# Kernel tuning notes

Measured on AMD Instinct MI355X. Metric: run time of the kernel, lower is better.

The kernel has to match this reference:

```python
import jax, jax.numpy as jnp
import numpy as np

B, T, H = 2, 2048, 1024
NH = 16
D = H // NH  # head_dim = 64
SCALE = D ** -0.5


def setup_inputs() -> dict:
    key = jax.random.key(0)
    ks = jax.random.split(key, 10)
    s_in = 1.0 / np.sqrt(H)   # torch Linear init scale for fan_in=H
    s_d = 1.0 / np.sqrt(D)
    return {
        "x":  jax.random.normal(ks[0], (B, T, H), jnp.float32),
        # stacked per-head Q/K projections: [NH, H, D] weights, [NH, D] biases
        "Wq": jax.random.uniform(ks[1], (NH, H, D), jnp.float32, -s_in, s_in),
        "bq": jax.random.uniform(ks[2], (NH, D), jnp.float32, -s_in, s_in),
        "Wk": jax.random.uniform(ks[3], (NH, H, D), jnp.float32, -s_in, s_in),
        "bk": jax.random.uniform(ks[4], (NH, D), jnp.float32, -s_in, s_in),
        # shared V projection H->D
        "Wv": jax.random.uniform(ks[5], (H, D), jnp.float32, -s_in, s_in),
        "bv": jax.random.uniform(ks[6], (D,), jnp.float32, -s_in, s_in),
        # out projection D->H
        "Wo": jax.random.uniform(ks[7], (D, H), jnp.float32, -s_d, s_d),
        "bo": jax.random.uniform(ks[8], (H,), jnp.float32, -s_d, s_d),
    }


def reference(x, Wq, bq, Wk, bk, Wv, bv, Wo, bo):
    # shared value projection: [B,T,D]
    v = jnp.einsum('bth,hd->btd', x, Wv) + bv
    # batched per-head Q/K projections: [NH,B,T,D]
    q = jnp.einsum('bth,nhd->nbtd', x, Wq) + bq[:, None, None, :]
    k = jnp.einsum('bth,nhd->nbtd', x, Wk) + bk[:, None, None, :]
    # scaled causal attention scores: [NH,B,T,T]
    scores = jnp.einsum('nbtd,nbsd->nbts', q, k) * SCALE
    causal = jnp.triu(jnp.ones((T, T), bool), k=1)  # True above diagonal
    scores = jnp.where(causal, -jnp.inf, scores)
    weights = jax.nn.softmax(scores, axis=-1)  # dropout is identity in eval
    # shared V attended per head, then mean over heads: [B,T,D]
    mean_head = jnp.einsum('nbts,bsd->btd', weights, v) / NH
    out = jnp.einsum('btd,dh->bth', mean_head, Wo) + bo
    mean_weights = jnp.mean(weights, axis=0)  # [B,T,T]
    return out, mean_weights
```

## Files before the change

### kernel.cpp

```cpp
#include <hip/hip_runtime.h>
#include <hip/hip_bf16.h>

#define B_ 2
#define T_ 2048
#define H_ 1024
#define NH_ 16
#define D_ 64
#define BT_ (B_*T_)
#define SCALE_ 0.125f
#define LOG2E_ 1.4426950408889634f

typedef _Float16 f16x8 __attribute__((ext_vector_type(8)));
typedef float f32x4 __attribute__((ext_vector_type(4)));

#define MFMA(a,b,c) __builtin_amdgcn_mfma_f32_16x16x32_f16((a),(b),(c),0,0,0)
#define EXP2(x) __builtin_amdgcn_exp2f(x)

typedef const __attribute__((address_space(1))) void GV;
typedef __attribute__((address_space(3))) void LV;

__device__ __forceinline__ size_t toff(int r, int c, int C) {
    return (size_t)((r >> 4) * (C >> 5) + (c >> 5)) * 512 + (size_t)(((c & 31) >> 3) * 128 + (r & 15) * 8 + (c & 7));
}
__device__ __forceinline__ f16x8 frag_ld(const _Float16* base, int rt, int kc, int Cc, int l15, int quad) {
    return *(const f16x8*)(base + (size_t)(rt * Cc + kc) * 512 + quad * 128 + l15 * 8);
}

__global__ __launch_bounds__(256) void k_prep(const float* __restrict__ x,
                                              const float* __restrict__ Wq, const float* __restrict__ Wk,
                                              const float* __restrict__ Wv, const float* __restrict__ Wo,
                                              _Float16* __restrict__ xb, _Float16* __restrict__ wqk,
                                              _Float16* __restrict__ wvt, _Float16* __restrict__ wot,
                                              float* __restrict__ mw) {
    int blk = blockIdx.x, tid = threadIdx.x;
    if (blk < 2048) {
        int idx = blk * 256 + tid;
        int t = idx >> 7, h0 = (idx & 127) * 8;
        const float* p = x + ((size_t)t << 10) + h0;
        float4 f0 = *(const float4*)p;
        float4 f1 = *(const float4*)(p + 4);
        f16x8 o;
        o[0]=(_Float16)f0.x; o[1]=(_Float16)f0.y; o[2]=(_Float16)f0.z; o[3]=(_Float16)f0.w;
        o[4]=(_Float16)f1.x; o[5]=(_Float16)f1.y; o[6]=(_Float16)f1.z; o[7]=(_Float16)f1.w;
        *(f16x8*)(xb + toff(t, h0, 1024)) = o;
    } else if (blk < 2560) {
        int idx = (blk - 2048) * 256 + tid;
        int head = idx >> 13;
        int rem = idx & 8191;
        int h = rem >> 3;
        int d0 = (rem & 7) * 8;
        const float* pq = Wq + ((size_t)((head << 10) + h)) * 64 + d0;
        const float* pk = Wk + ((size_t)((head << 10) + h)) * 64 + d0;
        float4 q0 = *(const float4*)pq, q1 = *(const float4*)(pq + 4);
        float4 k0 = *(const float4*)pk, k1 = *(const float4*)(pk + 4);
        float qv[8] = {q0.x,q0.y,q0.z,q0.w,q1.x,q1.y,q1.z,q1.w};
        float kv[8] = {k0.x,k0.y,k0.z,k0.w,k1.x,k1.y,k1.z,k1.w};
#pragma unroll
        for (int e = 0; e < 8; e++) {
            int c = head * 64 + d0 + e;
            wqk[toff(c, h, 1024)]        = (_Float16)qv[e];
            wqk[toff(c + 1024, h, 1024)] = (_Float16)kv[e];
        }
    } else if (blk < 2816) {
        int i = (blk - 2560) * 256 + tid;
        int d = i >> 10, h = i & 1023;
        wvt[toff(d, h, 1024)] = (_Float16)Wv[(size_t)h * 64 + d];
        int hh = i >> 6, dd = i & 63;
        wot[toff(hh, dd, 64)] = (_Float16)Wo[(size_t)dd * 1024 + hh];
    } else {
        int iz = blk - 2816;
        int b = (iz >= 496) ? 1 : 0;
        int i = iz - b * 496;
        int s64 = (int)((sqrtf(8.f * i + 1.f) + 1.f) * 0.5f);
        if (s64 * (s64 - 1) / 2 > i) s64--;
        if ((s64 + 1) * s64 / 2 <= i) s64++;
        int q64 = i - s64 * (s64 - 1) / 2;
        float4 z = {0.f, 0.f, 0.f, 0.f};
#pragma unroll
        for (int it = 0; it < 4; it++) {
            int idx = it * 256 + tid;
            int r = idx >> 4, c4 = idx & 15;
            *(float4*)&mw[(size_t)(b * T_ + q64 * 64 + r) * T_ + s64 * 64 + c4 * 4] = z;
        }
    }
}

__global__ __launch_bounds__(256) void k_gemm_qk(const _Float16* __restrict__ xb, const _Float16* __restrict__ wqk,
                                                 const float* __restrict__ bq, const float* __restrict__ bk,
                                                 _Float16* __restrict__ qh, _Float16* __restrict__ kh) {
    __shared__ __align__(16) _Float16 As[4096];
    __shared__ __align__(16) _Float16 Bs[4096];
    int bm = blockIdx.x >> 4, bn = blockIdx.x & 15;
    int tid = threadIdx.x, w = tid >> 6, lane = tid & 63, l15 = lane & 15, quad = lane >> 4;
    int rowbase = (w >> 1) * 64, colbase = (w & 1) * 64;
    f32x4 acc[4][4];
#pragma unroll
    for (int i = 0; i < 4; i++)
#pragma unroll
        for (int j = 0; j < 4; j++) acc[i][j] = (f32x4){0.f, 0.f, 0.f, 0.f};

    for (int kk = 0; kk < 32; kk++) {
        __syncthreads();
#pragma unroll
        for (int p = 0; p < 2; p++) {
            int c = w + p * 4;
            __builtin_amdgcn_global_load_lds((GV*)(xb  + ((size_t)((bm * 8 + c) * 32 + kk)) * 512 + lane * 8),
                                             (LV*)(As + c * 512 + lane * 8), 16, 0, 0);
            __builtin_amdgcn_global_load_lds((GV*)(wqk + ((size_t)((bn * 8 + c) * 32 + kk)) * 512 + lane * 8),
                                             (LV*)(Bs + c * 512 + lane * 8), 16, 0, 0);
        }
        __syncthreads();
        f16x8 a[4], bf[4];
#pragma unroll
        for (int i = 0; i < 4; i++) a[i]  = *(const f16x8*)&As[((rowbase >> 4) + i) * 512 + quad * 128 + l15 * 8];
#pragma unroll
        for (int j = 0; j < 4; j++) bf[j] = *(const f16x8*)&Bs[((colbase >> 4) + j) * 512 + quad * 128 + l15 * 8];
#pragma unroll
        for (int i = 0; i < 4; i++)
#pragma unroll
            for (int j = 0; j < 4; j++) acc[i][j] = MFMA(a[i], bf[j], acc[i][j]);
    }
    __syncthreads();
    int b = (bm * 128) >> 11;
    int t_base = (bm * 128) & 2047;
    int rtbase = (t_base + rowbase) >> 4;
    bool isq = (bn < 8);
    int c2base = isq ? (bn * 128 + colbase) : (bn * 128 + colbase - 1024);
    int n = c2base >> 6;
    _Float16* dst = (isq ? qh : kh) + (size_t)(n * 2 + b) * 131072;
    const float* bias_p = isq ? bq : bk;
    float qs = SCALE_ * LOG2E_;
    int i2 = lane >> 4, rowrb = lane & 15;
#pragma unroll
    for (int j = 0; j < 4; j++) {
        float bias = bias_p[c2base + j * 16 + l15];
        _Float16* stg = ((j & 1) ? Bs : As) + w * 1024;
#pragma unroll
        for (int i = 0; i < 4; i++)
#pragma unroll
            for (int r = 0; r < 4; r++) {
                float v = acc[i][j][r] + bias;
                if (isq) v *= qs;
                stg[(i * 16 + quad * 4 + r) * 16 + l15] = (_Float16)v;
            }
#pragma unroll
        for (int oct = 0; oct < 2; oct++) {
            f16x8 val = *(const f16x8*)&stg[(i2 * 16 + rowrb) * 16 + oct * 8];
            int dd0 = j * 16 + oct * 8;
            *(f16x8*)(dst + (size_t)((rtbase + i2) * 2 + (dd0 >> 5)) * 512 + ((dd0 & 31) >> 3) * 128 + rowrb * 8) = val;
        }
    }
}

__global__ __launch_bounds__(256) void k_vproj(const _Float16* __restrict__ xb, const _Float16* __restrict__ wvt,
                                               const float* __restrict__ bv, _Float16* __restrict__ vt) {
    __shared__ float red[4][16][64];
    int tid = threadIdx.x, w = tid >> 6, lane = tid & 63, l15 = lane & 15, quad = lane >> 4;
    int rt = blockIdx.x;
    f32x4 acc[4];
#pragma unroll
    for (int j = 0; j < 4; j++) acc[j] = (f32x4){0.f, 0.f, 0.f, 0.f};
    for (int q = 0; q < 8; q++) {
        int kc = w * 8 + q;
        f16x8 a = frag_ld(xb, rt, kc, 32, l15, quad);
#pragma unroll
        for (int j = 0; j < 4; j++) {
            f16x8 bb = frag_ld(wvt, j, kc, 32, l15, quad);
            acc[j] = MFMA(a, bb, acc[j]);
        }
    }
#pragma unroll
    for (int j = 0; j < 4; j++)
#pragma unroll
        for (int r = 0; r < 4; r++) red[w][quad * 4 + r][j * 16 + l15] = acc[j][r];
    __syncthreads();
    int r = tid >> 4, dg = tid & 15;
    int b = rt >> 7, tt = (rt & 127) * 16 + r;
    _Float16* vtb = vt + (size_t)b * 131072;
#pragma unroll
    for (int e = 0; e < 4; e++) {
        int d = dg * 4 + e;
        float s = red[0][r][d] + red[1][r][d] + red[2][r][d] + red[3][r][d] + bv[d];
        vtb[toff(d, tt, 2048)] = (_Float16)s;
    }
}

__global__ __launch_bounds__(256) void k_pass1(const _Float16* __restrict__ qh, const _Float16* __restrict__ kh,
                                               float* __restrict__ lstat4) {
    int tid = threadIdx.x, w = tid >> 6, lane = tid & 63, l15 = lane & 15, quad = lane >> 4;
    int blk = blockIdx.x;
    int n = blk >> 6, b = (blk >> 5) & 1, strip = blk & 31;
    const _Float16* qb = qh + (size_t)(n * 2 + b) * 131072;
    const _Float16* kp = kh + (size_t)(n * 2 + b) * 131072;
    int rt0 = strip * 4;
    f16x8 aq[4][2];
#pragma unroll
    for (int i = 0; i < 4; i++)
#pragma unroll
        for (int kk = 0; kk < 2; kk++) aq[i][kk] = frag_ld(qb, rt0 + i, kk, 2, l15, quad);
    float l[4][4];
#pragma unroll
    for (int i = 0; i < 4; i++)
#pragma unroll
        for (int r = 0; r < 4; r++) l[i][r] = 0.f;
    int st_lo = w * (strip + 1);
    int st_hi = st_lo + strip + 1;
    for (int st = st_lo; st < st_hi; st++) {
        f16x8 c0 = frag_ld(kp, st, 0, 2, l15, quad);
        f16x8 c1 = frag_ld(kp, st, 1, 2, l15, quad);
#pragma unroll
        for (int i = 0; i < 4; i++) {
            if (st > rt0 + i) continue;
            f32x4 sc = (f32x4){0.f, 0.f, 0.f, 0.f};
            sc = MFMA(aq[i][0], c0, sc);
            sc = MFMA(aq[i][1], c1, sc);
            if (st == rt0 + i) {
#pragma unroll
                for (int r = 0; r < 4; r++)
                    if (l15 <= quad * 4 + r) l[i][r] += EXP2(sc[r]);
            } else {
#pragma unroll
                for (int r = 0; r < 4; r++) l[i][r] += EXP2(sc[r]);
            }
        }
    }
#pragma unroll
    for (int off = 1; off < 16; off <<= 1)
#pragma unroll
        for (int i = 0; i < 4; i++)
#pragma unroll
            for (int r = 0; r < 4; r++) l[i][r] += __shfl_xor(l[i][r], off, 64);
    if (l15 == 0) {
        int base = (n * 2 + b) * 2048 + strip * 64;
#pragma unroll
        for (int i = 0; i < 4; i++)
#pragma unroll
            for (int r = 0; r < 4; r++)
                lstat4[(size_t)(base + i * 16 + quad * 4 + r) * 4 + w] = l[i][r];
    }
}

__global__ __launch_bounds__(256) void k_pass2o(const _Float16* __restrict__ qh, const _Float16* __restrict__ kh,
                                                const float* __restrict__ lstat4,
                                                float* __restrict__ mw, _Float16* __restrict__ mwh) {
    __shared__ float sl[16][128];
    __shared__ __align__(16) _Float16 kst[4096];
    int blk = blockIdx.x;
    int b = (blk >= 240) ? 1 : 0;
    int i0 = blk - 240 * b;
    int i = (i0 & 7) * 30 + (i0 >> 3);
    int p = (int)((1.f + sqrtf(4.f * i + 1.f)) * 0.5f);
    while (p * (p - 1) > i) p--;
    while (p * (p + 1) <= i) p++;
    int s64 = i - p * (p - 1);
    int tid = threadIdx.x, w = tid >> 6, lane = tid & 63, l15 = lane & 15, quad = lane >> 4;
    for (int ii = tid; ii < 2048; ii += 256) {
        int h = ii >> 7, r = ii & 127;
        const float4 pl = *(const float4*)&lstat4[(size_t)((h * 2 + b) * 2048 + p * 128 + r) * 4];
        sl[h][r] = 0.0625f / (pl.x + pl.y + pl.z + pl.w);
    }
    int rw = w * 32;
    int rt0 = (p * 128 + rw) >> 4;
    int st0 = s64 * 4;
    f32x4 macc[2][4];
#pragma unroll
    for (int ii = 0; ii < 2; ii++)
#pragma unroll
        for (int j = 0; j < 4; j++) macc[ii][j] = (f32x4){0.f, 0.f, 0.f, 0.f};

    for (int n = 0; n < NH_; n++) {
        const _Float16* qb = qh + (size_t)(n * 2 + b) * 131072;
        const _Float16* kp = kh + (size_t)(n * 2 + b) * 131072;
        __syncthreads();
#pragma unroll
        for (int inst = 0; inst < 2; inst++) {
            int c = inst * 4 + w;
            int gc = (st0 + (c >> 1)) * 2 + (c & 1);
            __builtin_amdgcn_global_load_lds((GV*)(kp + (size_t)gc * 512 + lane * 8),
                                             (LV*)(kst + c * 512 + lane * 8), 16, 0, 0);
        }
        f16x8 A[2][2];
#pragma unroll
        for (int ii = 0; ii < 2; ii++)
#pragma unroll
            for (int kc = 0; kc < 2; kc++) A[ii][kc] = frag_ld(qb, rt0 + ii, kc, 2, l15, quad);
        __syncthreads();
        f32x4 slv[2];
#pragma unroll
        for (int ii = 0; ii < 2; ii++) slv[ii] = *(const f32x4*)&sl[n][rw + ii * 16 + quad * 4];
#pragma unroll
        for (int j = 0; j < 4; j++) {
            f16x8 K0 = *(const f16x8*)&kst[(j * 2 + 0) * 512 + quad * 128 + l15 * 8];
            f16x8 K1 = *(const f16x8*)&kst[(j * 2 + 1) * 512 + quad * 128 + l15 * 8];
#pragma unroll
            for (int ii = 0; ii < 2; ii++) {
                f32x4 sc = (f32x4){0.f, 0.f, 0.f, 0.f};
                sc = MFMA(A[ii][0], K0, sc);
                sc = MFMA(A[ii][1], K1, sc);
#pragma unroll
                for (int r = 0; r < 4; r++) macc[ii][j][r] += EXP2(sc[r]) * slv[ii][r];
            }
        }
    }
    __syncthreads();
    float* mwb = mw + (size_t)b * T_ * T_;
#pragma unroll
    for (int ii = 0; ii < 2; ii++)
#pragma unroll
        for (int j = 0; j < 4; j++)
#pragma unroll
            for (int r = 0; r < 4; r++) {
                int tg = p * 128 + rw + ii * 16 + quad * 4 + r;
                int sg = s64 * 64 + j * 16 + l15;
                mwb[(size_t)tg * T_ + sg] = macc[ii][j][r];
            }
    _Float16* mhb = mwh + (size_t)b * 4194304;
    _Float16* ws16 = kst + w * 1024;
    int rowrb = lane & 15, qc = lane >> 4;
#pragma unroll
    for (int cc = 0; cc < 2; cc++) {
#pragma unroll
        for (int ii = 0; ii < 2; ii++)
#pragma unroll
            for (int j2 = 0; j2 < 2; j2++)
#pragma unroll
                for (int r = 0; r < 4; r++) {
                    int clw = j2 * 16 + l15;
                    ws16[ii * 512 + (clw >> 3) * 128 + (quad * 4 + r) * 8 + (clw & 7)] =
                        (_Float16)macc[ii][cc * 2 + j2][r];
                }
#pragma unroll
        for (int ii = 0; ii < 2; ii++) {
            f16x8 val = *(const f16x8*)&ws16[ii * 512 + qc * 128 + rowrb * 8];
            *(f16x8*)(mhb + (size_t)((rt0 + ii) * 64 + (s64 * 2 + cc)) * 512 + qc * 128 + rowrb * 8) = val;
        }
    }
}

__global__ __launch_bounds__(256) void k_pass2d(const _Float16* __restrict__ qh, const _Float16* __restrict__ kh,
                                                const float* __restrict__ lstat4,
                                                float* __restrict__ mw, _Float16* __restrict__ mwh) {
    int blk = blockIdx.x;
    int b = (blk >= 48) ? 1 : 0;
    int j0 = blk - 48 * b;
    int q64 = (j0 < 32) ? j0 : (2 * (j0 - 32) + 1);
    int s64 = (j0 < 32) ? j0 : (2 * (j0 - 32));
    int tid = threadIdx.x;
    __shared__ float sl[16][64];
    for (int ii = tid; ii < 1024; ii += 256) {
        int h = ii >> 6, r = ii & 63;
        const float4 p = *(const float4*)&lstat4[(size_t)((h * 2 + b) * 2048 + q64 * 64 + r) * 4];
        sl[h][r] = 0.0625f / (p.x + p.y + p.z + p.w);
    }
    __syncthreads();
    int w = tid >> 6, lane = tid & 63, l15 = lane & 15, quad = lane >> 4;
    int rw = (w >> 1) * 32, cw = (w & 1) * 32;
    int rt0 = (q64 * 64 + rw) >> 4, st0 = (s64 * 64 + cw) >> 4;
    f32x4 macc[2][2];
#pragma unroll
    for (int ii = 0; ii < 2; ii++)
#pragma unroll
        for (int j = 0; j < 2; j++) macc[ii][j] = (f32x4){0.f, 0.f, 0.f, 0.f};
#pragma unroll
    for (int n = 0; n < NH_; n++) {
        const _Float16* qb = qh + (size_t)(n * 2 + b) * 131072;
        const _Float16* kp = kh + (size_t)(n * 2 + b) * 131072;
        f16x8 aq[2][2], kb[2][2];
#pragma unroll
        for (int ii = 0; ii < 2; ii++)
#pragma unroll
            for (int kk = 0; kk < 2; kk++) {
                aq[ii][kk] = frag_ld(qb, rt0 + ii, kk, 2, l15, quad);
                kb[ii][kk] = frag_ld(kp, st0 + ii, kk, 2, l15, quad);
            }
        f32x4 slv[2];
#pragma unroll
        for (int ii = 0; ii < 2; ii++) slv[ii] = *(const f32x4*)&sl[n][rw + ii * 16 + quad * 4];
#pragma unroll
        for (int ii = 0; ii < 2; ii++)
#pragma unroll
            for (int j = 0; j < 2; j++) {
                f32x4 sc = (f32x4){0.f, 0.f, 0.f, 0.f};
                sc = MFMA(aq[ii][0], kb[j][0], sc);
                sc = MFMA(aq[ii][1], kb[j][1], sc);
                int sg = s64 * 64 + cw + j * 16 + l15;
#pragma unroll
                for (int r = 0; r < 4; r++) {
                    int tg = q64 * 64 + rw + ii * 16 + quad * 4 + r;
                    macc[ii][j][r] += (sg <= tg) ? EXP2(sc[r]) * slv[ii][r] : 0.f;
                }
            }
    }
    float* mwb = mw + (size_t)b * T_ * T_;
    _Float16* mhb = mwh + (size_t)b * 4194304;
#pragma unroll
    for (int ii = 0; ii < 2; ii++)
#pragma unroll
        for (int j = 0; j < 2; j++)
#pragma unroll
            for (int r = 0; r < 4; r++) {
                int tg = q64 * 64 + rw + ii * 16 + quad * 4 + r;
                int sg = s64 * 64 + cw + j * 16 + l15;
                float v = macc[ii][j][r];
                mwb[(size_t)tg * T_ + sg] = v;
                mhb[toff(tg, sg, 2048)] = (_Float16)v;
            }
}

__global__ __launch_bounds__(256) void k_pass3a(const _Float16* __restrict__ mwh, const _Float16* __restrict__ vt,
                                                _Float16* __restrict__ mhp) {
    __shared__ float red[4][16][64];
    int tid = threadIdx.x, w = tid >> 6, lane = tid & 63, l15 = lane & 15, quad = lane >> 4;
    int blk = blockIdx.x;
    int tile = blk >> 2, q = blk & 3;
    int b = tile >> 7, rtb = tile & 127;
    const _Float16* mb = mwh + (size_t)b * 4194304;
    const _Float16* vb = vt + (size_t)b * 131072;
    int nkc = (rtb * 16 + 47) >> 5;
    int qlo = q * 16;
    int qhi = min(qlo + 16, nkc);
    f32x4 acc[4];
#pragma unroll
    for (int j = 0; j < 4; j++) acc[j] = (f32x4){0.f, 0.f, 0.f, 0.f};
    for (int kc = qlo + w; kc < qhi; kc += 4) {
        f16x8 a = frag_ld(mb, rtb, kc, 64, l15, quad);
#pragma unroll
        for (int j = 0; j < 4; j++) {
            f16x8 bb = frag_ld(vb, j, kc, 64, l15, quad);
            acc[j] = MFMA(a, bb, acc[j]);
        }
    }
#pragma unroll
    for (int j = 0; j < 4; j++)
#pragma unroll
        for (int r = 0; r < 4; r++) red[w][quad * 4 + r][j * 16 + l15] = acc[j][r];
    __syncthreads();
    int r = tid >> 4, dg = tid & 15;
    _Float16* dst = mhp + (size_t)q * 262144;
#pragma unroll
    for (int e = 0; e < 4; e++) {
        int d = dg * 4 + e;
        float s = red[0][r][d] + red[1][r][d] + red[2][r][d] + red[3][r][d];
        dst[toff(tile * 16 + r, d, 64)] = (_Float16)s;
    }
}

__global__ __launch_bounds__(256) void k_pass3b(const _Float16* __restrict__ mhp, const _Float16* __restrict__ wot,
                                                const float* __restrict__ bo, float* __restrict__ out0) {
    int bm = blockIdx.x >> 4, bn = blockIdx.x & 15;
    int tid = threadIdx.x, w = tid >> 6, lane = tid & 63, l15 = lane & 15, quad = lane >> 4;
    int rt = bm * 4 + w;
    f16x8 a0[4], a1[4];
#pragma unroll
    for (int q = 0; q < 4; q++) {
        const _Float16* mb = mhp + (size_t)q * 262144;
        a0[q] = frag_ld(mb, rt, 0, 2, l15, quad);
        a1[q] = frag_ld(mb, rt, 1, 2, l15, quad);
    }
    f32x4 acc[4];
#pragma unroll
    for (int j = 0; j < 4; j++) acc[j] = (f32x4){0.f, 0.f, 0.f, 0.f};
#pragma unroll
    for (int j = 0; j < 4; j++) {
        f16x8 b0 = frag_ld(wot, bn * 4 + j, 0, 2, l15, quad);
        f16x8 b1 = frag_ld(wot, bn * 4 + j, 1, 2, l15, quad);
#pragma unroll
        for (int q = 0; q < 4; q++) {
            acc[j] = MFMA(a0[q], b0, acc[j]);
            acc[j] = MFMA(a1[q], b1, acc[j]);
        }
    }
#pragma unroll
    for (int j = 0; j < 4; j++)
#pragma unroll
        for (int r = 0; r < 4; r++) {
            int row = rt * 16 + quad * 4 + r;
            int col = bn * 64 + j * 16 + l15;
            out0[(size_t)row * 1024 + col] = acc[j][r] + bo[col];
        }
}

extern "C" void kernel_launch(void* const* d_in, const int* in_sizes, int n_in,
                              void* d_out, int out_size, void* d_ws, size_t ws_size,
                              hipStream_t stream) {
    const float* x  = (const float*)d_in[0];
    const float* Wq = (const float*)d_in[1];
    const float* bq = (const float*)d_in[2];
    const float* Wk = (const float*)d_in[3];
    const float* bk = (const float*)d_in[4];
    const float* Wv = (const float*)d_in[5];
    const float* bv = (const float*)d_in[6];
    const float* Wo = (const float*)d_in[7];
    const float* bo = (const float*)d_in[8];
    char* ws = (char*)d_ws;
    _Float16* xb    = (_Float16*)(ws + 0);
    _Float16* wqk   = (_Float16*)(ws + 8388608);
    _Float16* wvt   = (_Float16*)(ws + 12582912);
    _Float16* mwh   = (_Float16*)(ws + 0);
    _Float16* qh    = (_Float16*)(ws + 16777216);
    _Float16* kh    = (_Float16*)(ws + 25165824);
    _Float16* vt    = (_Float16*)(ws + 33554432);
    float*    lstat4= (float*)   (ws + 34078720);
    _Float16* mhp   = (_Float16*)(ws + 35127296);
    _Float16* wot   = (_Float16*)(ws + 37224448);
    float* out0 = (float*)d_out;
    float* mw   = out0 + (size_t)BT_ * H_;

    k_prep    <<<3808, 256, 0, stream>>>(x, Wq, Wk, Wv, Wo, xb, wqk, wvt, wot, mw);
    k_gemm_qk <<<512,  256, 0, stream>>>(xb, wqk, bq, bk, qh, kh);
    k_vproj   <<<256,  256, 0, stream>>>(xb, wvt, bv, vt);
    k_pass1   <<<1024, 256, 0, stream>>>(qh, kh, lstat4);
    k_pass2o  <<<480,  256, 0, stream>>>(qh, kh, lstat4, mw, mwh);
    k_pass2d  <<<96,   256, 0, stream>>>(qh, kh, lstat4, mw, mwh);
    k_pass3a  <<<1024, 256, 0, stream>>>(mwh, vt, mhp);
    k_pass3b  <<<1024, 256, 0, stream>>>(mhp, wot, bo, out0);
}
```

Measured before the change: 219.8 us.

## Merge V projection into QK GEMM, unify pass2 kernels with double-buffered K

Folds the V projection into the QK GEMM launch as extra blocks, and deepens the GEMM K-step so each iteration loads two k-chunks per barrier. Replaces the separate off-diagonal and diagonal pass2 kernels with one kernel over 128x64 tiles. Diagonal tiles take a masked path, and the next head's K tile and Q fragments are prefetched into a double-buffered LDS while the current head computes. This removes two launches and exposes load latency to overlap, at the cost of more LDS per block and a divergent branch for masked tiles.

```diff
diff --git a/kernel.cpp b/kernel.cpp
--- a/kernel.cpp
+++ b/kernel.cpp
@@ -85,13 +85,47 @@
     }
 }
 
-__global__ __launch_bounds__(256) void k_gemm_qk(const _Float16* __restrict__ xb, const _Float16* __restrict__ wqk,
-                                                 const float* __restrict__ bq, const float* __restrict__ bk,
-                                                 _Float16* __restrict__ qh, _Float16* __restrict__ kh) {
-    __shared__ __align__(16) _Float16 As[4096];
-    __shared__ __align__(16) _Float16 Bs[4096];
+__global__ __launch_bounds__(256) void k_gemm(const _Float16* __restrict__ xb, const _Float16* __restrict__ wqk,
+                                              const float* __restrict__ bq, const float* __restrict__ bk,
+                                              const _Float16* __restrict__ wvt, const float* __restrict__ bv,
+                                              _Float16* __restrict__ qh, _Float16* __restrict__ kh,
+                                              _Float16* __restrict__ vt) {
+    __shared__ __align__(16) unsigned char smem[32768];
+    _Float16* As = (_Float16*)smem;
+    _Float16* Bs = (_Float16*)(smem + 16384);
+    int tid = threadIdx.x, w = tid >> 6, lane = tid & 63, l15 = lane & 15, quad = lane >> 4;
+    if (blockIdx.x >= 512) {
+        float (*red)[16][64] = (float(*)[16][64])smem;
+        int rt = blockIdx.x - 512;
+        f32x4 acc[4];
+#pragma unroll
+        for (int j = 0; j < 4; j++) acc[j] = (f32x4){0.f, 0.f, 0.f, 0.f};
+        for (int q = 0; q < 8; q++) {
+            int kc = w * 8 + q;
+            f16x8 a = frag_ld(xb, rt, kc, 32, l15, quad);
+#pragma unroll
+            for (int j = 0; j < 4; j++) {
+                f16x8 bb = frag_ld(wvt, j, kc, 32, l15, quad);
+                acc[j] = MFMA(a, bb, acc[j]);
+            }
+        }
+#pragma unroll
+        for (int j = 0; j < 4; j++)
+#pragma unroll
+            for (int r = 0; r < 4; r++) red[w][quad * 4 + r][j * 16 + l15] = acc[j][r];
+        __syncthreads();
+        int r = tid >> 4, dg = tid & 15;
+        int b = rt >> 7, tt = (rt & 127) * 16 + r;
+        _Float16* vtb = vt + (size_t)b * 131072;
+#pragma unroll
+        for (int e = 0; e < 4; e++) {
+            int d = dg * 4 + e;
+            float s = red[0][r][d] + red[1][r][d] + red[2][r][d] + red[3][r][d] + bv[d];
+            vtb[toff(d, tt, 2048)] = (_Float16)s;
+        }
+        return;
+    }
     int bm = blockIdx.x >> 4, bn = blockIdx.x & 15;
-    int tid = threadIdx.x, w = tid >> 6, lane = tid & 63, l15 = lane & 15, quad = lane >> 4;
     int rowbase = (w >> 1) * 64, colbase = (w & 1) * 64;
     f32x4 acc[4][4];
 #pragma unroll
@@ -99,26 +133,29 @@
 #pragma unroll
         for (int j = 0; j < 4; j++) acc[i][j] = (f32x4){0.f, 0.f, 0.f, 0.f};
 
-    for (int kk = 0; kk < 32; kk++) {
+    for (int kk = 0; kk < 16; kk++) {
         __syncthreads();
 #pragma unroll
-        for (int p = 0; p < 2; p++) {
-            int c = w + p * 4;
-            __builtin_amdgcn_global_load_lds((GV*)(xb  + ((size_t)((bm * 8 + c) * 32 + kk)) * 512 + lane * 8),
+        for (int p = 0; p < 4; p++) {
+            int c = w * 4 + p;
+            __builtin_amdgcn_global_load_lds((GV*)(xb  + ((size_t)((bm * 8 + (c >> 1)) * 32 + kk * 2 + (c & 1))) * 512 + lane * 8),
                                              (LV*)(As + c * 512 + lane * 8), 16, 0, 0);
-            __builtin_amdgcn_global_load_lds((GV*)(wqk + ((size_t)((bn * 8 + c) * 32 + kk)) * 512 + lane * 8),
+            __builtin_amdgcn_global_load_lds((GV*)(wqk + ((size_t)((bn * 8 + (c >> 1)) * 32 + kk * 2 + (c & 1))) * 512 + lane * 8),
                                              (LV*)(Bs + c * 512 + lane * 8), 16, 0, 0);
         }
         __syncthreads();
-        f16x8 a[4], bf[4];
-#pragma unroll
-        for (int i = 0; i < 4; i++) a[i]  = *(const f16x8*)&As[((rowbase >> 4) + i) * 512 + quad * 128 + l15 * 8];
-#pragma unroll
-        for (int j = 0; j < 4; j++) bf[j] = *(const f16x8*)&Bs[((colbase >> 4) + j) * 512 + quad * 128 + l15 * 8];
-#pragma unroll
-        for (int i = 0; i < 4; i++)
-#pragma unroll
-            for (int j = 0; j < 4; j++) acc[i][j] = MFMA(a[i], bf[j], acc[i][j]);
+#pragma unroll
+        for (int kc = 0; kc < 2; kc++) {
+            f16x8 a[4], bf[4];
+#pragma unroll
+            for (int i = 0; i < 4; i++) a[i]  = *(const f16x8*)&As[((rowbase >> 4) + i) * 1024 + kc * 512 + quad * 128 + l15 * 8];
+#pragma unroll
+            for (int j = 0; j < 4; j++) bf[j] = *(const f16x8*)&Bs[((colbase >> 4) + j) * 1024 + kc * 512 + quad * 128 + l15 * 8];
+#pragma unroll
+            for (int i = 0; i < 4; i++)
+#pragma unroll
+                for (int j = 0; j < 4; j++) acc[i][j] = MFMA(a[i], bf[j], acc[i][j]);
+        }
     }
     __syncthreads();
     int b = (bm * 128) >> 11;
@@ -152,39 +189,6 @@
     }
 }
 
-__global__ __launch_bounds__(256) void k_vproj(const _Float16* __restrict__ xb, const _Float16* __restrict__ wvt,
-                                               const float* __restrict__ bv, _Float16* __restrict__ vt) {
-    __shared__ float red[4][16][64];
-    int tid = threadIdx.x, w = tid >> 6, lane = tid & 63, l15 = lane & 15, quad = lane >> 4;
-    int rt = blockIdx.x;
-    f32x4 acc[4];
-#pragma unroll
-    for (int j = 0; j < 4; j++) acc[j] = (f32x4){0.f, 0.f, 0.f, 0.f};
-    for (int q = 0; q < 8; q++) {
-        int kc = w * 8 + q;
-        f16x8 a = frag_ld(xb, rt, kc, 32, l15, quad);
-#pragma unroll
-        for (int j = 0; j < 4; j++) {
-            f16x8 bb = frag_ld(wvt, j, kc, 32, l15, quad);
-            acc[j] = MFMA(a, bb, acc[j]);
-        }
-    }
-#pragma unroll
-    for (int j = 0; j < 4; j++)
-#pragma unroll
-        for (int r = 0; r < 4; r++) red[w][quad * 4 + r][j * 16 + l15] = acc[j][r];
-    __syncthreads();
-    int r = tid >> 4, dg = tid & 15;
-    int b = rt >> 7, tt = (rt & 127) * 16 + r;
-    _Float16* vtb = vt + (size_t)b * 131072;
-#pragma unroll
-    for (int e = 0; e < 4; e++) {
-        int d = dg * 4 + e;
-        float s = red[0][r][d] + red[1][r][d] + red[2][r][d] + red[3][r][d] + bv[d];
-        vtb[toff(d, tt, 2048)] = (_Float16)s;
-    }
-}
-
 __global__ __launch_bounds__(256) void k_pass1(const _Float16* __restrict__ qh, const _Float16* __restrict__ kh,
                                                float* __restrict__ lstat4) {
     int tid = threadIdx.x, w = tid >> 6, lane = tid & 63, l15 = lane & 15, quad = lane >> 4;
@@ -240,19 +244,20 @@
     }
 }
 
-__global__ __launch_bounds__(256) void k_pass2o(const _Float16* __restrict__ qh, const _Float16* __restrict__ kh,
-                                                const float* __restrict__ lstat4,
-                                                float* __restrict__ mw, _Float16* __restrict__ mwh) {
+__global__ __launch_bounds__(256) void k_pass2(const _Float16* __restrict__ qh, const _Float16* __restrict__ kh,
+                                               const float* __restrict__ lstat4,
+                                               float* __restrict__ mw, _Float16* __restrict__ mwh) {
     __shared__ float sl[16][128];
-    __shared__ __align__(16) _Float16 kst[4096];
+    __shared__ __align__(16) _Float16 kst[2][4096];
     int blk = blockIdx.x;
-    int b = (blk >= 240) ? 1 : 0;
-    int i0 = blk - 240 * b;
-    int i = (i0 & 7) * 30 + (i0 >> 3);
-    int p = (int)((1.f + sqrtf(4.f * i + 1.f)) * 0.5f);
-    while (p * (p - 1) > i) p--;
-    while (p * (p + 1) <= i) p++;
-    int s64 = i - p * (p - 1);
+    int b = (blk >= 272) ? 1 : 0;
+    int i0 = blk - 272 * b;
+    int i = (i0 & 7) * 34 + (i0 >> 3);
+    int p = (int)((sqrtf(4.f * i + 1.f) - 1.f) * 0.5f);
+    while (p * (p + 1) > i) p--;
+    while ((p + 1) * (p + 2) <= i) p++;
+    int s64 = i - p * (p + 1);
+    bool masked = (s64 >= 2 * p);
     int tid = threadIdx.x, w = tid >> 6, lane = tid & 63, l15 = lane & 15, quad = lane >> 4;
     for (int ii = tid; ii < 2048; ii += 256) {
         int h = ii >> 7, r = ii & 127;
@@ -260,7 +265,7 @@
         sl[h][r] = 0.0625f / (pl.x + pl.y + pl.z + pl.w);
     }
     int rw = w * 32;
-    int rt0 = (p * 128 + rw) >> 4;
+    int rt0 = p * 8 + w * 2;
     int st0 = s64 * 4;
     f32x4 macc[2][4];
 #pragma unroll
@@ -268,41 +273,72 @@
 #pragma unroll
         for (int j = 0; j < 4; j++) macc[ii][j] = (f32x4){0.f, 0.f, 0.f, 0.f};
 
-    for (int n = 0; n < NH_; n++) {
-        const _Float16* qb = qh + (size_t)(n * 2 + b) * 131072;
-        const _Float16* kp = kh + (size_t)(n * 2 + b) * 131072;
-        __syncthreads();
+    {
+        const _Float16* kp = kh + (size_t)b * 131072;
 #pragma unroll
         for (int inst = 0; inst < 2; inst++) {
             int c = inst * 4 + w;
             int gc = (st0 + (c >> 1)) * 2 + (c & 1);
             __builtin_amdgcn_global_load_lds((GV*)(kp + (size_t)gc * 512 + lane * 8),
-                                             (LV*)(kst + c * 512 + lane * 8), 16, 0, 0);
-        }
-        f16x8 A[2][2];
+                                             (LV*)(kst[0] + c * 512 + lane * 8), 16, 0, 0);
+        }
+    }
+    f16x8 An[2][2];
+#pragma unroll
+    for (int ii = 0; ii < 2; ii++)
+#pragma unroll
+        for (int kc = 0; kc < 2; kc++) An[ii][kc] = frag_ld(qh + (size_t)b * 131072, rt0 + ii, kc, 2, l15, quad);
+    __syncthreads();
+
+    for (int n = 0; n < NH_; n++) {
+        f16x8 Ac[2][2];
 #pragma unroll
         for (int ii = 0; ii < 2; ii++)
 #pragma unroll
-            for (int kc = 0; kc < 2; kc++) A[ii][kc] = frag_ld(qb, rt0 + ii, kc, 2, l15, quad);
-        __syncthreads();
+            for (int kc = 0; kc < 2; kc++) Ac[ii][kc] = An[ii][kc];
+        if (n < NH_ - 1) {
+            const _Float16* kp = kh + (size_t)((n + 1) * 2 + b) * 131072;
+            const _Float16* qb = qh + (size_t)((n + 1) * 2 + b) * 131072;
+#pragma unroll
+            for (int inst = 0; inst < 2; inst++) {
+                int c = inst * 4 + w;
+                int gc = (st0 + (c >> 1)) * 2 + (c & 1);
+                __builtin_amdgcn_global_load_lds((GV*)(kp + (size_t)gc * 512 + lane * 8),
+                                                 (LV*)(kst[(n + 1) & 1] + c * 512 + lane * 8), 16, 0, 0);
+            }
+#pragma unroll
+            for (int ii = 0; ii < 2; ii++)
+#pragma unroll
+                for (int kc = 0; kc < 2; kc++) An[ii][kc] = frag_ld(qb, rt0 + ii, kc, 2, l15, quad);
+        }
         f32x4 slv[2];
 #pragma unroll
         for (int ii = 0; ii < 2; ii++) slv[ii] = *(const f32x4*)&sl[n][rw + ii * 16 + quad * 4];
+        const _Float16* ks = kst[n & 1];
 #pragma unroll
         for (int j = 0; j < 4; j++) {
-            f16x8 K0 = *(const f16x8*)&kst[(j * 2 + 0) * 512 + quad * 128 + l15 * 8];
-            f16x8 K1 = *(const f16x8*)&kst[(j * 2 + 1) * 512 + quad * 128 + l15 * 8];
+            f16x8 K0 = *(const f16x8*)&ks[(j * 2 + 0) * 512 + quad * 128 + l15 * 8];
+            f16x8 K1 = *(const f16x8*)&ks[(j * 2 + 1) * 512 + quad * 128 + l15 * 8];
 #pragma unroll
             for (int ii = 0; ii < 2; ii++) {
                 f32x4 sc = (f32x4){0.f, 0.f, 0.f, 0.f};
-                sc = MFMA(A[ii][0], K0, sc);
-                sc = MFMA(A[ii][1], K1, sc);
-#pragma unroll
-                for (int r = 0; r < 4; r++) macc[ii][j][r] += EXP2(sc[r]) * slv[ii][r];
-            }
-        }
-    }
-    __syncthreads();
+                sc = MFMA(Ac[ii][0], K0, sc);
+                sc = MFMA(Ac[ii][1], K1, sc);
+                if (masked) {
+                    int sg = s64 * 64 + j * 16 + l15;
+#pragma unroll
+                    for (int r = 0; r < 4; r++) {
+                        int tg = p * 128 + rw + ii * 16 + quad * 4 + r;
+                        macc[ii][j][r] += (sg <= tg) ? EXP2(sc[r]) * slv[ii][r] : 0.f;
+                    }
+                } else {
+#pragma unroll
+                    for (int r = 0; r < 4; r++) macc[ii][j][r] += EXP2(sc[r]) * slv[ii][r];
+                }
+            }
+        }
+        __syncthreads();
+    }
     float* mwb = mw + (size_t)b * T_ * T_;
 #pragma unroll
     for (int ii = 0; ii < 2; ii++)
@@ -315,7 +351,7 @@
                 mwb[(size_t)tg * T_ + sg] = macc[ii][j][r];
             }
     _Float16* mhb = mwh + (size_t)b * 4194304;
-    _Float16* ws16 = kst + w * 1024;
+    _Float16* ws16 = kst[0] + w * 1024;
     int rowrb = lane & 15, qc = lane >> 4;
 #pragma unroll
     for (int cc = 0; cc < 2; cc++) {
@@ -335,76 +371,6 @@
             *(f16x8*)(mhb + (size_t)((rt0 + ii) * 64 + (s64 * 2 + cc)) * 512 + qc * 128 + rowrb * 8) = val;
         }
     }
-}
-
-__global__ __launch_bounds__(256) void k_pass2d(const _Float16* __restrict__ qh, const _Float16* __restrict__ kh,
-                                                const float* __restrict__ lstat4,
-                                                float* __restrict__ mw, _Float16* __restrict__ mwh) {
-    int blk = blockIdx.x;
-    int b = (blk >= 48) ? 1 : 0;
-    int j0 = blk - 48 * b;
-    int q64 = (j0 < 32) ? j0 : (2 * (j0 - 32) + 1);
-    int s64 = (j0 < 32) ? j0 : (2 * (j0 - 32));
-    int tid = threadIdx.x;
-    __shared__ float sl[16][64];
-    for (int ii = tid; ii < 1024; ii += 256) {
-        int h = ii >> 6, r = ii & 63;
-        const float4 p = *(const float4*)&lstat4[(size_t)((h * 2 + b) * 2048 + q64 * 64 + r) * 4];
-        sl[h][r] = 0.0625f / (p.x + p.y + p.z + p.w);
-    }
-    __syncthreads();
-    int w = tid >> 6, lane = tid & 63, l15 = lane & 15, quad = lane >> 4;
-    int rw = (w >> 1) * 32, cw = (w & 1) * 32;
-    int rt0 = (q64 * 64 + rw) >> 4, st0 = (s64 * 64 + cw) >> 4;
-    f32x4 macc[2][2];
-#pragma unroll
-    for (int ii = 0; ii < 2; ii++)
-#pragma unroll
-        for (int j = 0; j < 2; j++) macc[ii][j] = (f32x4){0.f, 0.f, 0.f, 0.f};
-#pragma unroll
-    for (int n = 0; n < NH_; n++) {
-        const _Float16* qb = qh + (size_t)(n * 2 + b) * 131072;
-        const _Float16* kp = kh + (size_t)(n * 2 + b) * 131072;
-        f16x8 aq[2][2], kb[2][2];
-#pragma unroll
-        for (int ii = 0; ii < 2; ii++)
-#pragma unroll
-            for (int kk = 0; kk < 2; kk++) {
-                aq[ii][kk] = frag_ld(qb, rt0 + ii, kk, 2, l15, quad);
-                kb[ii][kk] = frag_ld(kp, st0 + ii, kk, 2, l15, quad);
-            }
-        f32x4 slv[2];
-#pragma unroll
-        for (int ii = 0; ii < 2; ii++) slv[ii] = *(const f32x4*)&sl[n][rw + ii * 16 + quad * 4];
-#pragma unroll
-        for (int ii = 0; ii < 2; ii++)
-#pragma unroll
-            for (int j = 0; j < 2; j++) {
-                f32x4 sc = (f32x4){0.f, 0.f, 0.f, 0.f};
-                sc = MFMA(aq[ii][0], kb[j][0], sc);
-                sc = MFMA(aq[ii][1], kb[j][1], sc);
-                int sg = s64 * 64 + cw + j * 16 + l15;
-#pragma unroll
-                for (int r = 0; r < 4; r++) {
-                    int tg = q64 * 64 + rw + ii * 16 + quad * 4 + r;
-                    macc[ii][j][r] += (sg <= tg) ? EXP2(sc[r]) * slv[ii][r] : 0.f;
-                }
-            }
-    }
-    float* mwb = mw + (size_t)b * T_ * T_;
-    _Float16* mhb = mwh + (size_t)b * 4194304;
-#pragma unroll
-    for (int ii = 0; ii < 2; ii++)
-#pragma unroll
-        for (int j = 0; j < 2; j++)
-#pragma unroll
-            for (int r = 0; r < 4; r++) {
-                int tg = q64 * 64 + rw + ii * 16 + quad * 4 + r;
-                int sg = s64 * 64 + cw + j * 16 + l15;
-                float v = macc[ii][j][r];
-                mwb[(size_t)tg * T_ + sg] = v;
-                mhb[toff(tg, sg, 2048)] = (_Float16)v;
-            }
 }
 
 __global__ __launch_bounds__(256) void k_pass3a(const _Float16* __restrict__ mwh, const _Float16* __restrict__ vt,
@@ -506,12 +472,10 @@
     float* out0 = (float*)d_out;
     float* mw   = out0 + (size_t)BT_ * H_;
 
-    k_prep    <<<3808, 256, 0, stream>>>(x, Wq, Wk, Wv, Wo, xb, wqk, wvt, wot, mw);
-    k_gemm_qk <<<512,  256, 0, stream>>>(xb, wqk, bq, bk, qh, kh);
-    k_vproj   <<<256,  256, 0, stream>>>(xb, wvt, bv, vt);
-    k_pass1   <<<1024, 256, 0, stream>>>(qh, kh, lstat4);
-    k_pass2o  <<<480,  256, 0, stream>>>(qh, kh, lstat4, mw, mwh);
-    k_pass2d  <<<96,   256, 0, stream>>>(qh, kh, lstat4, mw, mwh);
-    k_pass3a  <<<1024, 256, 0, stream>>>(mwh, vt, mhp);
-    k_pass3b  <<<1024, 256, 0, stream>>>(mhp, wot, bo, out0);
-}
+    k_prep   <<<3808, 256, 0, stream>>>(x, Wq, Wk, Wv, Wo, xb, wqk, wvt, wot, mw);
+    k_gemm   <<<768,  256, 0, stream>>>(xb, wqk, bq, bk, wvt, bv, qh, kh, vt);
+    k_pass1  <<<1024, 256, 0, stream>>>(qh, kh, lstat4);
+    k_pass2  <<<544,  256, 0, stream>>>(qh, kh, lstat4, mw, mwh);
+    k_pass3a <<<1024, 256, 0, stream>>>(mwh, vt, mhp);
+    k_pass3b <<<1024, 256, 0, stream>>>(mhp, wot, bo, out0);
+}
```

Result: faster. 208.9 us (-5.0%).
